# Kernel tuning notes

Hardware: AMD Instinct MI355X
Metric: run time of the kernel (lower is better)

Reference implementation:

```python
import jax, jax.numpy as jnp
import numpy as np
import math

B, S, D, H, R = 4, 2048, 512, 8, 8  # R = k+1 relative slots per direction


def setup_inputs() -> dict:
    key = jax.random.key(0)
    ks = jax.random.split(key, 16)
    dk = D // H
    sc = 1.0 / math.sqrt(D)
    return {
        "query": jax.random.normal(ks[0], (B, S, D), jnp.float32),
        "key": jax.random.normal(ks[1], (B, S, D), jnp.float32),
        "value": jax.random.normal(ks[2], (B, S, D), jnp.float32),
        "start_nodes": jax.random.randint(ks[3], (B, H, R, S), 0, S, jnp.int64 if jax.config.jax_enable_x64 else jnp.int32),
        "end_nodes": jax.random.randint(ks[4], (B, H, R, S), 0, S, jnp.int64 if jax.config.jax_enable_x64 else jnp.int32),
        "rel_q": jax.random.normal(ks[5], (1, H, 2 * R, dk), jnp.float32),
        "rel_k": jax.random.normal(ks[6], (1, H, 2 * R, dk), jnp.float32),
        "rel_v": jax.random.normal(ks[7], (1, H, 2 * R, dk), jnp.float32),
        "Wq": jax.random.normal(ks[8], (D, D), jnp.float32) * sc,
        "bq": jnp.zeros((D,), jnp.float32),
        "Wk": jax.random.normal(ks[9], (D, D), jnp.float32) * sc,
        "bk": jnp.zeros((D,), jnp.float32),
        "Wv": jax.random.normal(ks[10], (D, D), jnp.float32) * sc,
        "bv": jnp.zeros((D,), jnp.float32),
        "Wo": jax.random.normal(ks[11], (D, D), jnp.float32) * sc,
        "bo": jnp.zeros((D,), jnp.float32),
    }


def reference(query, key, value, start_nodes, end_nodes, rel_q, rel_k, rel_v,
              Wq, bq, Wk, bk, Wv, bv, Wo, bo):
    Bs, Ss, Ds = query.shape
    Hs = start_nodes.shape[1]
    dk = Ds // Hs

    def proj(x, W, b):
        return (x @ W.T + b).reshape(Bs, Ss, Hs, dk).transpose(0, 2, 1, 3)  # [B,H,S,dk]

    q = proj(query, Wq, bq)
    k = proj(key, Wk, bk)
    v = proj(value, Wv, bv)

    start_mask = start_nodes == -1
    sn = jnp.where(start_mask, 0, start_nodes)  # -1 padding -> 0 (masked out below)
    qidx = jnp.concatenate([end_nodes, sn], axis=2)  # [B,H,2R,S]
    kidx = jnp.concatenate([sn, end_nodes], axis=2)

    bi = jnp.arange(Bs)[:, None, None, None]
    hi = jnp.arange(Hs)[None, :, None, None]
    q_ctx = q[bi, hi, qidx]  # [B,H,2R,S,dk]
    k_ctx = k[bi, hi, kidx]
    v_ctx = v[bi, hi, kidx]

    # c2c + c2p + p2c, scale_factor = 3 (rel_q and rel_k both provided)
    scores = ((q_ctx * k_ctx).sum(-1)
              + (q_ctx * rel_k[:, :, :, None, :]).sum(-1)
              + (rel_q[:, :, :, None, :] * k_ctx).sum(-1))
    scores = scores / (3.0 * jnp.sqrt(jnp.asarray(dk, scores.dtype)))

    # mask: padded edges masked in both halves; first S flat entries always masked
    mask = jnp.concatenate([start_mask, start_mask], axis=2).reshape(Bs, Hs, -1)
    mask = mask.at[:, :, :Ss].set(True)
    sflat = jnp.exp(jnp.where(mask, -1e9, scores.reshape(Bs, Hs, -1)))  # [B,H,2R*S]

    qf = qidx.reshape(Bs, Hs, -1)
    b2 = jnp.arange(Bs)[:, None, None]
    h2 = jnp.arange(Hs)[None, :, None]
    # scatter-add softmax denominator over destination nodes, then gather back
    denom = jnp.zeros((Bs, Hs, Ss), sflat.dtype).at[b2, h2, qf].add(sflat)
    denom = jnp.where(denom == 0, -1e9, denom)
    probs = (sflat / denom[b2, h2, qf]).reshape(Bs, Hs, -1, Ss, 1)  # [B,H,2R,S,1]

    attn_v = probs * (v_ctx + rel_v[:, :, :, None, :])  # [B,H,2R,S,dk]
    out = jnp.zeros((Bs, Hs, Ss, dk), attn_v.dtype).at[b2, h2, qf].add(
        attn_v.reshape(Bs, Hs, -1, dk))  # scatter-add aggregation over edges

    out = out.transpose(0, 2, 1, 3).reshape(Bs, Ss, Ds)
    return out @ Wo.T + bo
```

## Files before the change

### kernel.cpp

```cpp
#include <hip/hip_runtime.h>
#include <math.h>

#define B_ 4
#define S_ 2048
#define D_ 512
#define H_ 8
#define R_ 8
#define DK_ 64
#define NEDGE (B_*H_*2*R_*S_)
#define EPB   (2*R_*S_)
#define ELLCAP 64

typedef __attribute__((ext_vector_type(8))) short bf16x8;
typedef __attribute__((ext_vector_type(8))) unsigned short ushort8_t;
typedef __attribute__((ext_vector_type(4))) float f32x4;

#define AS1q const __attribute__((address_space(1)))
#define AS3q __attribute__((address_space(3)))

__device__ inline unsigned short f2bf(float f) {
    unsigned u = __builtin_bit_cast(unsigned, f);
    u += 0x7fffu + ((u >> 16) & 1u);
    return (unsigned short)(u >> 16);
}
__device__ inline float bf2f(unsigned short u) {
    return __builtin_bit_cast(float, ((unsigned)u) << 16);
}

__global__ __launch_bounds__(256) void prep(
    const float* __restrict__ query, const float* __restrict__ key,
    const float* __restrict__ value,
    const float* __restrict__ Wq, const float* __restrict__ Wk,
    const float* __restrict__ Wv, const float* __restrict__ Wo,
    const float* __restrict__ rel_q, const float* __restrict__ rel_k,
    const float* __restrict__ rel_v,
    unsigned short* __restrict__ qc, unsigned short* __restrict__ kc,
    unsigned short* __restrict__ vc,
    unsigned short* __restrict__ wqb, unsigned short* __restrict__ wkb,
    unsigned short* __restrict__ wvb, unsigned short* __restrict__ wob,
    unsigned short* __restrict__ rqb, unsigned short* __restrict__ rkb,
    unsigned short* __restrict__ rvb)
{
    int bid = blockIdx.x;
    const float* x;
    unsigned short* y;
    size_t i;
    if (bid < 12288) {
        int z = bid >> 12;
        x = (z == 0) ? query : (z == 1) ? key : value;
        y = (z == 0) ? qc : (z == 1) ? kc : vc;
        i = ((size_t)(bid & 4095) * 256 + threadIdx.x) * 4;
    } else if (bid < 13312) {
        int r = bid - 12288;
        int z = r >> 8;
        x = (z == 0) ? Wq : (z == 1) ? Wk : (z == 2) ? Wv : Wo;
        y = (z == 0) ? wqb : (z == 1) ? wkb : (z == 2) ? wvb : wob;
        i = ((size_t)(r & 255) * 256 + threadIdx.x) * 4;
    } else {
        int r = bid - 13312;
        int z = r >> 3;
        x = (z == 0) ? rel_q : (z == 1) ? rel_k : rel_v;
        y = (z == 0) ? rqb : (z == 1) ? rkb : rvb;
        i = ((size_t)(r & 7) * 256 + threadIdx.x) * 4;
    }
    float4 v = *(const float4*)&x[i];
    *(ushort4*)&y[i] = make_ushort4(f2bf(v.x), f2bf(v.y), f2bf(v.z), f2bf(v.w));
}

template<int TN>
__global__ __launch_bounds__(256) void gemm_bf16(
    const unsigned short* __restrict__ A0, const unsigned short* __restrict__ A1,
    const unsigned short* __restrict__ A2,
    const unsigned short* __restrict__ W0, const unsigned short* __restrict__ W1,
    const unsigned short* __restrict__ W2,
    const float* __restrict__ bi0, const float* __restrict__ bi1, const float* __restrict__ bi2,
    unsigned short* __restrict__ C0, unsigned short* __restrict__ C1,
    unsigned short* __restrict__ C2,
    float* __restrict__ Cf, int a_bhsd)
{
    constexpr int NFR = TN / 32;
    __shared__ unsigned short As[128 * 64];
    __shared__ unsigned short Bs[TN * 64];
    const int z = blockIdx.z;
    const unsigned short* A = (z == 0) ? A0 : (z == 1) ? A1 : A2;
    const unsigned short* W = (z == 0) ? W0 : (z == 1) ? W1 : W2;
    const float* bias        = (z == 0) ? bi0 : (z == 1) ? bi1 : bi2;
    unsigned short* C        = (z == 0) ? C0 : (z == 1) ? C1 : C2;

    const int t    = threadIdx.x;
    const int lane = t & 63;
    const int w    = t >> 6;
    const int wm   = w >> 1, wn = w & 1;
    const int m0   = blockIdx.x * 128;
    const int n0   = blockIdx.y * TN;

    const int lr    = lane >> 3;
    const int cglob = (lane & 7) ^ lr;

    f32x4 acc[4][NFR] = {};

    for (int kk = 0; kk < D_; kk += 64) {
        #pragma unroll
        for (int i = 0; i < 4; ++i) {
            int rowl = w * 32 + i * 8;
            int m = m0 + rowl + lr;
            const unsigned short* ga;
            if (a_bhsd) {
                int b = m >> 11, s = m & (S_ - 1), h = kk >> 6;
                ga = A + ((((size_t)b * H_ + h) * S_ + s) << 6) + cglob * 8;
            } else {
                ga = A + (size_t)m * D_ + kk + cglob * 8;
            }
            __builtin_amdgcn_global_load_lds((AS1q unsigned*)ga,
                (AS3q unsigned*)(As + rowl * 64), 16, 0, 0);
        }
        #pragma unroll
        for (int i = 0; i < TN / 32; ++i) {
            int rowl = w * (TN / 4) + i * 8;
            const unsigned short* gb =
                W + (size_t)(n0 + rowl + lr) * D_ + kk + cglob * 8;
            __builtin_amdgcn_global_load_lds((AS1q unsigned*)gb,
                (AS3q unsigned*)(Bs + rowl * 64), 16, 0, 0);
        }
        __syncthreads();

        #pragma unroll
        for (int ks = 0; ks < 64; ks += 32) {
            const int c0 = ks >> 3;
            bf16x8 af[4], bfr[NFR];
            #pragma unroll
            for (int mi = 0; mi < 4; ++mi) {
                int row = wm * 64 + mi * 16 + (lane & 15);
                int cp  = (c0 + (lane >> 4)) ^ (lane & 7);
                af[mi] = *(const bf16x8*)&As[row * 64 + cp * 8];
            }
            #pragma unroll
            for (int nj = 0; nj < NFR; ++nj) {
                int row = wn * (TN / 2) + nj * 16 + (lane & 15);
                int cp  = (c0 + (lane >> 4)) ^ (lane & 7);
                bfr[nj] = *(const bf16x8*)&Bs[row * 64 + cp * 8];
            }
            #pragma unroll
            for (int mi = 0; mi < 4; ++mi)
                #pragma unroll
                for (int nj = 0; nj < NFR; ++nj)
                    acc[mi][nj] = __builtin_amdgcn_mfma_f32_16x16x32_bf16(af[mi], bfr[nj], acc[mi][nj], 0, 0, 0);
        }
        __syncthreads();
    }

    #pragma unroll
    for (int mi = 0; mi < 4; ++mi) {
        #pragma unroll
        for (int nj = 0; nj < NFR; ++nj) {
            #pragma unroll
            for (int r = 0; r < 4; ++r) {
                int m = m0 + wm * 64 + mi * 16 + (lane >> 4) * 4 + r;
                int n = n0 + wn * (TN / 2) + nj * 16 + (lane & 15);
                float val = acc[mi][nj][r] + bias[n];
                if (Cf) {
                    Cf[(size_t)m * D_ + n] = val;
                } else {
                    int b = m >> 11, s = m & (S_ - 1);
                    int h = n >> 6,  d = n & 63;
                    C[((((size_t)b * H_ + h) * S_ + s) << 6) + d] = f2bf(val);
                }
            }
        }
    }
}

__global__ __launch_bounds__(1024) void build_ell(
    const int* __restrict__ start_nodes, const int* __restrict__ end_nodes,
    int* __restrict__ deg, unsigned short* __restrict__ ell)
{
    __shared__ int cnt[256];
    const int bh  = blockIdx.x >> 3;
    const int oct = blockIdx.x & 7;
    const int t   = threadIdx.x;
    const int dlo = oct << 8;
    if (t < 256) cnt[t] = 0;
    __syncthreads();

    const int base_idx = bh * (R_ * S_);
    for (int f = t; f < EPB; f += 1024) {
        int r2 = f >> 11;
        if (r2 == 0) continue;
        int s = f & (S_ - 1);
        int r = r2 & 7;
        int idx = base_idx + r * S_ + s;
        int sn = start_nodes[idx];
        if (sn == -1) continue;
        int en = end_nodes[idx];
        int dst = (r2 < R_) ? en : sn;
        unsigned rel = (unsigned)(dst - dlo);
        if (rel < 256u) {
            int ki = (r2 < R_) ? sn : en;
            int pos = atomicAdd(&cnt[rel], 1);
            if (pos < ELLCAP)
                ell[((size_t)(bh * S_ + dst)) * ELLCAP + pos] =
                    (unsigned short)((r2 << 11) | ki);
        }
    }
    __syncthreads();
    if (t < 256) deg[bh * S_ + dlo + t] = cnt[t];
}

__global__ __launch_bounds__(256) void edge_gather(
    const unsigned short* __restrict__ q, const unsigned short* __restrict__ k_,
    const unsigned short* __restrict__ v_,
    const unsigned short* __restrict__ rel_q, const unsigned short* __restrict__ rel_k,
    const unsigned short* __restrict__ rel_v,
    const int* __restrict__ deg, const unsigned short* __restrict__ ell,
    unsigned short* __restrict__ attn)
{
    int raw = blockIdx.x;
    int xcd = raw & 7;
    int loc = raw >> 3;
    int bh  = xcd * 4 + (loc >> 9);
    int wid = threadIdx.x >> 6;
    int dst = (loc & 511) * 4 + wid;
    int lane = threadIdx.x & 63;
    int grp = lane >> 3;
    int sub = lane & 7;
    int h = bh & 7;
    int g = bh * S_ + dst;
    size_t node_base = ((size_t)bh << 11);

    ushort8_t q8 = *(const ushort8_t*)&q[((node_base + dst) << 6) + sub * 8];
    float qv[8];
    #pragma unroll
    for (int i = 0; i < 8; ++i) qv[i] = bf2f(q8[i]);

    int n = deg[g];
    if (n > ELLCAP) n = ELLCAP;
    int d_all = (int)ell[(size_t)g * ELLCAP + lane];

    float den = 0.f;
    float o[8] = {};
    #pragma unroll 2
    for (int j = 0; j < n; j += 8) {
        int slot = j + grp;
        int d = __shfl(d_all, slot);
        bool valid = slot < n;
        int ki = d & (S_ - 1);
        int r2 = (d >> 11) & 15;
        ushort8_t k8  = *(const ushort8_t*)&k_  [((node_base + ki) << 6) + sub * 8];
        ushort8_t rk8 = *(const ushort8_t*)&rel_k[(((h << 4) + r2) << 6) + sub * 8];
        ushort8_t rq8 = *(const ushort8_t*)&rel_q[(((h << 4) + r2) << 6) + sub * 8];
        float p = 0.f;
        #pragma unroll
        for (int i = 0; i < 8; ++i)
            p = fmaf(bf2f(k8[i]), qv[i] + bf2f(rq8[i]),
                     fmaf(qv[i], bf2f(rk8[i]), p));
        p += __shfl_xor(p, 1);
        p += __shfl_xor(p, 2);
        p += __shfl_xor(p, 4);
        float sf = valid ? __expf(p * (1.0f / 24.0f)) : 0.f;
        ushort8_t v8  = *(const ushort8_t*)&v_  [((node_base + ki) << 6) + sub * 8];
        ushort8_t rv8 = *(const ushort8_t*)&rel_v[(((h << 4) + r2) << 6) + sub * 8];
        den += sf;
        #pragma unroll
        for (int i = 0; i < 8; ++i)
            o[i] = fmaf(sf, bf2f(v8[i]) + bf2f(rv8[i]), o[i]);
    }
    den += __shfl_xor(den, 8); den += __shfl_xor(den, 16); den += __shfl_xor(den, 32);
    #pragma unroll
    for (int i = 0; i < 8; ++i) {
        o[i] += __shfl_xor(o[i], 8);
        o[i] += __shfl_xor(o[i], 16);
        o[i] += __shfl_xor(o[i], 32);
    }
    if (grp == 0) {
        float inv = (den > 0.f) ? 1.0f / den : 0.f;
        ushort8_t r;
        #pragma unroll
        for (int i = 0; i < 8; ++i) r[i] = f2bf(o[i] * inv);
        *(ushort8_t*)&attn[((node_base + dst) << 6) + sub * 8] = r;
    }
}

extern "C" void kernel_launch(void* const* d_in, const int* in_sizes, int n_in,
                              void* d_out, int out_size, void* d_ws, size_t ws_size,
                              hipStream_t stream) {
    const float* query = (const float*)d_in[0];
    const float* key   = (const float*)d_in[1];
    const float* value = (const float*)d_in[2];
    const int* start_nodes = (const int*)d_in[3];
    const int* end_nodes   = (const int*)d_in[4];
    const float* rel_q = (const float*)d_in[5];
    const float* rel_k = (const float*)d_in[6];
    const float* rel_v = (const float*)d_in[7];
    const float* Wq = (const float*)d_in[8];
    const float* bq = (const float*)d_in[9];
    const float* Wk = (const float*)d_in[10];
    const float* bk = (const float*)d_in[11];
    const float* Wv = (const float*)d_in[12];
    const float* bv = (const float*)d_in[13];
    const float* Wo = (const float*)d_in[14];
    const float* bo = (const float*)d_in[15];
    float* out = (float*)d_out;

    const size_t NQ = (size_t)B_ * H_ * S_ * DK_;
    const size_t NW = (size_t)D_ * D_;
    const size_t NR = (size_t)H_ * 2 * R_ * DK_;
    const size_t NG = (size_t)B_ * H_ * S_;
    unsigned short* p = (unsigned short*)d_ws;
    unsigned short* qc = p;            p += NQ;
    unsigned short* kc = p;            p += NQ;
    unsigned short* vc = p;            p += NQ;
    unsigned short* q  = p;            p += NQ;
    unsigned short* k  = p;            p += NQ;
    unsigned short* v  = p;            p += NQ;
    unsigned short* attn = p;          p += NQ;
    unsigned short* wqb = p;           p += NW;
    unsigned short* wkb = p;           p += NW;
    unsigned short* wvb = p;           p += NW;
    unsigned short* wob = p;           p += NW;
    unsigned short* rqb = p;           p += NR;
    unsigned short* rkb = p;           p += NR;
    unsigned short* rvb = p;           p += NR;
    unsigned short* ell = p;           p += NG * ELLCAP;
    int* deg = (int*)p;

    prep<<<13336, 256, 0, stream>>>(query, key, value, Wq, Wk, Wv, Wo,
                                    rel_q, rel_k, rel_v,
                                    qc, kc, vc, wqb, wkb, wvb, wob,
                                    rqb, rkb, rvb);

    build_ell<<<B_ * H_ * 8, 1024, 0, stream>>>(start_nodes, end_nodes, deg, ell);

    dim3 ggrid(B_ * S_ / 128, D_ / 128, 3);
    gemm_bf16<128><<<ggrid, 256, 0, stream>>>(qc, kc, vc, wqb, wkb, wvb, bq, bk, bv,
                                              q, k, v, nullptr, 0);

    edge_gather<<<(B_ * H_ * S_) / 4, 256, 0, stream>>>(
        q, k, v, rqb, rkb, rvb, deg, ell, attn);

    dim3 ogrid(B_ * S_ / 128, D_ / 64, 1);
    gemm_bf16<64><<<ogrid, 256, 0, stream>>>(attn, attn, attn, wob, wob, wob, bo, bo, bo,
                                             nullptr, nullptr, nullptr, out, 1);
}
```

Baseline: 237.6 us.

## Fuse ELL construction into edge gather kernel using shared-memory adjacency

Merges the build_ell and edge_gather kernels into one kernel. Each 1024-thread block builds the adjacency list for 128 destination nodes in LDS and then aggregates them. This removes the global ELL/degree buffers and a kernel launch. In exchange, each block rescans the whole edge list of its batch-head, doubling redundant index reads, and the gather phase runs with far fewer blocks and serial per-wave destination loops.

Result: faster. 218.8 us (-7.9%).

```diff
diff --git a/kernel.cpp b/kernel.cpp
--- a/kernel.cpp
+++ b/kernel.cpp
@@ -170,16 +170,24 @@
     }
 }
 
-__global__ __launch_bounds__(1024) void build_ell(
+__global__ __launch_bounds__(1024) void attn_fused(
+    const unsigned short* __restrict__ q, const unsigned short* __restrict__ k_,
+    const unsigned short* __restrict__ v_,
+    const unsigned short* __restrict__ rel_q, const unsigned short* __restrict__ rel_k,
+    const unsigned short* __restrict__ rel_v,
     const int* __restrict__ start_nodes, const int* __restrict__ end_nodes,
-    int* __restrict__ deg, unsigned short* __restrict__ ell)
+    unsigned short* __restrict__ attn)
 {
-    __shared__ int cnt[256];
-    const int bh  = blockIdx.x >> 3;
-    const int oct = blockIdx.x & 7;
+    __shared__ unsigned short ell[128 * ELLCAP];
+    __shared__ int cnt[128];
+    const int bi  = blockIdx.x;
+    const int xcd = bi & 7;
+    const int loc = bi >> 3;
+    const int bh  = xcd * 4 + (loc >> 4);
+    const int dlo = (loc & 15) << 7;
     const int t   = threadIdx.x;
-    const int dlo = oct << 8;
-    if (t < 256) cnt[t] = 0;
+
+    if (t < 128) cnt[t] = 0;
     __syncthreads();
 
     const int base_idx = bh * (R_ * S_);
@@ -187,96 +195,83 @@
         int r2 = f >> 11;
         if (r2 == 0) continue;
         int s = f & (S_ - 1);
-        int r = r2 & 7;
-        int idx = base_idx + r * S_ + s;
+        int idx = base_idx + (r2 & 7) * S_ + s;
         int sn = start_nodes[idx];
         if (sn == -1) continue;
         int en = end_nodes[idx];
         int dst = (r2 < R_) ? en : sn;
         unsigned rel = (unsigned)(dst - dlo);
-        if (rel < 256u) {
+        if (rel < 128u) {
             int ki = (r2 < R_) ? sn : en;
             int pos = atomicAdd(&cnt[rel], 1);
             if (pos < ELLCAP)
-                ell[((size_t)(bh * S_ + dst)) * ELLCAP + pos] =
-                    (unsigned short)((r2 << 11) | ki);
+                ell[(rel << 6) + pos] = (unsigned short)((r2 << 11) | ki);
         }
     }
     __syncthreads();
-    if (t < 256) deg[bh * S_ + dlo + t] = cnt[t];
-}
-
-__global__ __launch_bounds__(256) void edge_gather(
-    const unsigned short* __restrict__ q, const unsigned short* __restrict__ k_,
-    const unsigned short* __restrict__ v_,
-    const unsigned short* __restrict__ rel_q, const unsigned short* __restrict__ rel_k,
-    const unsigned short* __restrict__ rel_v,
-    const int* __restrict__ deg, const unsigned short* __restrict__ ell,
-    unsigned short* __restrict__ attn)
-{
-    int raw = blockIdx.x;
-    int xcd = raw & 7;
-    int loc = raw >> 3;
-    int bh  = xcd * 4 + (loc >> 9);
-    int wid = threadIdx.x >> 6;
-    int dst = (loc & 511) * 4 + wid;
-    int lane = threadIdx.x & 63;
-    int grp = lane >> 3;
-    int sub = lane & 7;
-    int h = bh & 7;
-    int g = bh * S_ + dst;
-    size_t node_base = ((size_t)bh << 11);
-
-    ushort8_t q8 = *(const ushort8_t*)&q[((node_base + dst) << 6) + sub * 8];
-    float qv[8];
-    #pragma unroll
-    for (int i = 0; i < 8; ++i) qv[i] = bf2f(q8[i]);
-
-    int n = deg[g];
-    if (n > ELLCAP) n = ELLCAP;
-    int d_all = (int)ell[(size_t)g * ELLCAP + lane];
-
-    float den = 0.f;
-    float o[8] = {};
-    #pragma unroll 2
-    for (int j = 0; j < n; j += 8) {
-        int slot = j + grp;
-        int d = __shfl(d_all, slot);
-        bool valid = slot < n;
-        int ki = d & (S_ - 1);
-        int r2 = (d >> 11) & 15;
-        ushort8_t k8  = *(const ushort8_t*)&k_  [((node_base + ki) << 6) + sub * 8];
-        ushort8_t rk8 = *(const ushort8_t*)&rel_k[(((h << 4) + r2) << 6) + sub * 8];
-        ushort8_t rq8 = *(const ushort8_t*)&rel_q[(((h << 4) + r2) << 6) + sub * 8];
-        float p = 0.f;
-        #pragma unroll
-        for (int i = 0; i < 8; ++i)
-            p = fmaf(bf2f(k8[i]), qv[i] + bf2f(rq8[i]),
-                     fmaf(qv[i], bf2f(rk8[i]), p));
-        p += __shfl_xor(p, 1);
-        p += __shfl_xor(p, 2);
-        p += __shfl_xor(p, 4);
-        float sf = valid ? __expf(p * (1.0f / 24.0f)) : 0.f;
-        ushort8_t v8  = *(const ushort8_t*)&v_  [((node_base + ki) << 6) + sub * 8];
-        ushort8_t rv8 = *(const ushort8_t*)&rel_v[(((h << 4) + r2) << 6) + sub * 8];
-        den += sf;
-        #pragma unroll
-        for (int i = 0; i < 8; ++i)
-            o[i] = fmaf(sf, bf2f(v8[i]) + bf2f(rv8[i]), o[i]);
-    }
-    den += __shfl_xor(den, 8); den += __shfl_xor(den, 16); den += __shfl_xor(den, 32);
-    #pragma unroll
-    for (int i = 0; i < 8; ++i) {
-        o[i] += __shfl_xor(o[i], 8);
-        o[i] += __shfl_xor(o[i], 16);
-        o[i] += __shfl_xor(o[i], 32);
-    }
-    if (grp == 0) {
-        float inv = (den > 0.f) ? 1.0f / den : 0.f;
-        ushort8_t r;
-        #pragma unroll
-        for (int i = 0; i < 8; ++i) r[i] = f2bf(o[i] * inv);
-        *(ushort8_t*)&attn[((node_base + dst) << 6) + sub * 8] = r;
+
+    const int w    = t >> 6;
+    const int lane = t & 63;
+    const int grp  = lane >> 3;
+    const int sub  = lane & 7;
+    const int h    = bh & 7;
+    const size_t node_base = ((size_t)bh << 11);
+
+    for (int dd = 0; dd < 8; ++dd) {
+        int dl  = dd * 16 + w;
+        int dst = dlo + dl;
+
+        ushort8_t q8 = *(const ushort8_t*)&q[((node_base + dst) << 6) + sub * 8];
+        float qv[8];
+        #pragma unroll
+        for (int i = 0; i < 8; ++i) qv[i] = bf2f(q8[i]);
+
+        int n = cnt[dl];
+        if (n > ELLCAP) n = ELLCAP;
+        int d_all = (int)ell[(dl << 6) + lane];
+
+        float den = 0.f;
+        float o[8] = {};
+        #pragma unroll 2
+        for (int j = 0; j < n; j += 8) {
+            int slot = j + grp;
+            int d = __shfl(d_all, slot);
+            bool valid = slot < n;
+            int ki = d & (S_ - 1);
+            int r2 = (d >> 11) & 15;
+            ushort8_t k8  = *(const ushort8_t*)&k_  [((node_base + ki) << 6) + sub * 8];
+            ushort8_t rk8 = *(const ushort8_t*)&rel_k[(((h << 4) + r2) << 6) + sub * 8];
+            ushort8_t rq8 = *(const ushort8_t*)&rel_q[(((h << 4) + r2) << 6) + sub * 8];
+            float p = 0.f;
+            #pragma unroll
+            for (int i = 0; i < 8; ++i)
+                p = fmaf(bf2f(k8[i]), qv[i] + bf2f(rq8[i]),
+                         fmaf(qv[i], bf2f(rk8[i]), p));
+            p += __shfl_xor(p, 1);
+            p += __shfl_xor(p, 2);
+            p += __shfl_xor(p, 4);
+            float sf = valid ? __expf(p * (1.0f / 24.0f)) : 0.f;
+            ushort8_t v8  = *(const ushort8_t*)&v_  [((node_base + ki) << 6) + sub * 8];
+            ushort8_t rv8 = *(const ushort8_t*)&rel_v[(((h << 4) + r2) << 6) + sub * 8];
+            den += sf;
+            #pragma unroll
+            for (int i = 0; i < 8; ++i)
+                o[i] = fmaf(sf, bf2f(v8[i]) + bf2f(rv8[i]), o[i]);
+        }
+        den += __shfl_xor(den, 8); den += __shfl_xor(den, 16); den += __shfl_xor(den, 32);
+        #pragma unroll
+        for (int i = 0; i < 8; ++i) {
+            o[i] += __shfl_xor(o[i], 8);
+            o[i] += __shfl_xor(o[i], 16);
+            o[i] += __shfl_xor(o[i], 32);
+        }
+        if (grp == 0) {
+            float inv = (den > 0.f) ? 1.0f / den : 0.f;
+            ushort8_t r;
+            #pragma unroll
+            for (int i = 0; i < 8; ++i) r[i] = f2bf(o[i] * inv);
+            *(ushort8_t*)&attn[((node_base + dst) << 6) + sub * 8] = r;
+        }
     }
 }
 
@@ -304,7 +299,6 @@
     const size_t NQ = (size_t)B_ * H_ * S_ * DK_;
     const size_t NW = (size_t)D_ * D_;
     const size_t NR = (size_t)H_ * 2 * R_ * DK_;
-    const size_t NG = (size_t)B_ * H_ * S_;
     unsigned short* p = (unsigned short*)d_ws;
     unsigned short* qc = p;            p += NQ;
     unsigned short* kc = p;            p += NQ;
@@ -320,22 +314,18 @@
     unsigned short* rqb = p;           p += NR;
     unsigned short* rkb = p;           p += NR;
     unsigned short* rvb = p;           p += NR;
-    unsigned short* ell = p;           p += NG * ELLCAP;
-    int* deg = (int*)p;
 
     prep<<<13336, 256, 0, stream>>>(query, key, value, Wq, Wk, Wv, Wo,
                                     rel_q, rel_k, rel_v,
                                     qc, kc, vc, wqb, wkb, wvb, wob,
                                     rqb, rkb, rvb);
 
-    build_ell<<<B_ * H_ * 8, 1024, 0, stream>>>(start_nodes, end_nodes, deg, ell);
-
     dim3 ggrid(B_ * S_ / 128, D_ / 128, 3);
     gemm_bf16<128><<<ggrid, 256, 0, stream>>>(qc, kc, vc, wqb, wkb, wvb, bq, bk, bv,
                                               q, k, v, nullptr, 0);
 
-    edge_gather<<<(B_ * H_ * S_) / 4, 256, 0, stream>>>(
-        q, k, v, rqb, rkb, rvb, deg, ell, attn);
+    attn_fused<<<512, 1024, 0, stream>>>(q, k, v, rqb, rkb, rvb,
+                                         start_nodes, end_nodes, attn);
 
     dim3 ogrid(B_ * S_ / 128, D_ / 64, 1);
     gemm_bf16<64><<<ogrid, 256, 0, stream>>>(attn, attn, attn, wob, wob, wob, bo, bo, bo,
```
